# Kernel tuning notes

Measured on AMD Instinct MI355X. Metric: run time of the kernel, lower is better.

Reference implementation:

```python
import jax, jax.numpy as jnp
import numpy as np

B, N, DIM = 2, 512, 512
HEADS, DIM_HEAD, MAX_LEN = 8, 64, 1024


def _skew(QEr):
    # pad last dim on the left by 1, reshape (n, n+1) -> (n+1, n), drop first row
    padded = jnp.pad(QEr, ((0, 0), (0, 0), (0, 0), (1, 0)))
    b, h, r, c = padded.shape
    return padded.reshape(b, h, c, r)[:, :, 1:, :]


def _fft_multiply_parallel(A, x):
    # A: [b,h,n,n] decay matrix; x: [b,h,n,d]
    b, h, n, d = x.shape
    # y = [last column of A, first row of A] -> [b,h,2n]
    y = jnp.concatenate([A[:, :, :, -1], A[:, :, 0, :]], axis=-1)
    v = jnp.concatenate([x, jnp.zeros_like(x)], axis=-2)  # zero-pad rows n -> 2n
    # Faithful to the original torch code: fftn over ALL axes (incl. batch/head),
    # then ifft over the LAST axis only, then slice back to n rows.
    H = jnp.fft.fftn(y)[:, :, :, None] * jnp.fft.fftn(v)
    return jnp.fft.ifft(H)[:, :, :n, :]


def _forward(x, Wq, Wk, Wv, Er):
    b, n, _ = x.shape

    def split_heads(t):
        return t.reshape(b, n, HEADS, DIM_HEAD).transpose(0, 2, 1, 3)  # [b,h,n,d]

    q = split_heads(x @ Wq)
    k = split_heads(x @ Wk)
    v = split_heads(x @ Wv)
    # global (Frobenius) norm over the full tensor, as torch.norm(t)
    q = q / jnp.linalg.norm(q)
    k = k / jnp.linalg.norm(k)
    q_ = jax.nn.elu(q)
    k_ = jax.nn.elu(k)

    Er_t = Er[MAX_LEN - n:, :].T        # [d, n]
    QEr = q @ Er_t                       # [b,h,n,n]
    c = jnp.exp(_skew(QEr))              # relative-position decay, [b,h,n,n]

    a_1 = jnp.einsum('bhnx,bhny->bhnxy', k_, v).reshape(b, HEADS, n, DIM_HEAD * DIM_HEAD)
    d_2 = _fft_multiply_parallel(c, k_)                                   # [b,h,n,d] complex
    d_1 = _fft_multiply_parallel(c, a_1).reshape(b, HEADS, n, DIM_HEAD, DIM_HEAD)

    top = jnp.einsum('bhnx,bhnyz->bhnz', q_, d_1)    # complex [b,h,n,d]
    bottom = jnp.einsum('bhnx,bhny->bhny', q_, d_2)  # complex [b,h,n,d]
    return top / bottom


def setup_inputs() -> dict:
    key = jax.random.key(0)
    k1, k2, k3, k4, k5 = jax.random.split(key, 5)
    s = jnp.float32(1.0 / np.sqrt(DIM))
    return {
        'x': jax.random.normal(k1, (B, N, DIM), dtype=jnp.float32),
        'Wq': jax.random.normal(k2, (DIM, HEADS * DIM_HEAD), dtype=jnp.float32) * s,
        'Wk': jax.random.normal(k3, (DIM, HEADS * DIM_HEAD), dtype=jnp.float32) * s,
        'Wv': jax.random.normal(k4, (DIM, HEADS * DIM_HEAD), dtype=jnp.float32) * s,
        'Er': jax.random.normal(k5, (MAX_LEN, DIM_HEAD), dtype=jnp.float32),
    }


def reference(x, Wq, Wk, Wv, Er):
    return _forward(x, Wq, Wk, Wv, Er)
```

## Files before the change

### kernel.cpp

```cpp
#include <hip/hip_runtime.h>
#include <math.h>


#define DIMX 512
#define NPOS 512
#define PADIDX(m) ((m) + ((m) >> 4))

typedef unsigned short ushort_t;
typedef unsigned int uint_t;
typedef __bf16 bf16x8 __attribute__((ext_vector_type(8)));
typedef float floatx4 __attribute__((ext_vector_type(4)));

static __device__ inline ushort_t f2bf(float f) {
    uint_t u = __float_as_uint(f);
    u = u + 0x7FFFu + ((u >> 16) & 1u);
    return (ushort_t)(u >> 16);
}
static __device__ inline float bf2f(ushort_t h) {
    return __uint_as_float(((uint_t)h) << 16);
}

#define BFLY(lo, hi, tw) do {                                   \
    const float sr_ = (lo).x - (hi).x, si_ = (lo).y - (hi).y;   \
    (lo).x += (hi).x; (lo).y += (hi).y;                         \
    (hi).x = sr_ * (tw).x - si_ * (tw).y;                       \
    (hi).y = sr_ * (tw).y + si_ * (tw).x;                       \
} while (0)

__global__ __launch_bounds__(256)
void conv_kernel(const float* __restrict__ x,
                 const float* __restrict__ Wk, const float* __restrict__ Wv,
                 ushort_t* __restrict__ xh, ushort_t* __restrict__ xl,
                 ushort_t* __restrict__ wth, ushort_t* __restrict__ wtl,
                 float2* __restrict__ twd)
{
    const int blk = blockIdx.x;
    const int t = threadIdx.x;
    if (blk < 512) {
        const int idx4 = blk * 256 + t;
        const float4 v = ((const float4*)x)[idx4];
        const float vf[4] = {v.x, v.y, v.z, v.w};
        ushort_t h[4], l[4];
        #pragma unroll
        for (int e = 0; e < 4; ++e) {
            h[e] = f2bf(vf[e]);
            l[e] = f2bf(vf[e] - bf2f(h[e]));
        }
        ushort_t* ph = xh + (size_t)idx4 * 4;
        ushort_t* pl = xl + (size_t)idx4 * 4;
        #pragma unroll
        for (int e = 0; e < 4; ++e) { ph[e] = h[e]; pl[e] = l[e]; }
    } else if (blk < 1024) {
        __shared__ float tile[32][33];
        const int b2 = blk - 512;
        const int s  = b2 >> 8;
        const int kt = (b2 >> 4) & 15;
        const int nt = b2 & 15;
        const int c  = t & 31, r4 = t >> 5;
        const float* __restrict__ W = s ? Wv : Wk;
        #pragma unroll
        for (int i = 0; i < 4; ++i) {
            const int row = r4 + i * 8;
            tile[row][c] = W[(size_t)(kt * 32 + row) * 512 + nt * 32 + c];
        }
        __syncthreads();
        #pragma unroll
        for (int i = 0; i < 4; ++i) {
            const int nl = r4 + i * 8;
            const float v = tile[c][nl];
            const ushort_t h = f2bf(v);
            const ushort_t l = f2bf(v - bf2f(h));
            const size_t o = (size_t)(s * 512 + nt * 32 + nl) * 512 + kt * 32 + c;
            wth[o] = h;
            wtl[o] = l;
        }
    } else {
        const int jj = (blk - 1024) * 256 + t;
        double s, cc;
        sincos(-6.2831853071795864769 * (double)jj / 1024.0, &s, &cc);
        twd[jj] = make_float2((float)cc, (float)s);
    }
}

__global__ __launch_bounds__(256)
void gemm_mfma_kernel(const ushort_t* __restrict__ xh, const ushort_t* __restrict__ xl,
                      const ushort_t* __restrict__ wth, const ushort_t* __restrict__ wtl,
                      float* __restrict__ K, float* __restrict__ V,
                      float* __restrict__ partials)
{
    const int blk = blockIdx.x;
    const int ct = blk >> 5;
    const int rt = blk & 31;
    const int t = threadIdx.x;
    const int w = t >> 6, lane = t & 63;
    const int qd = lane >> 4, lm = lane & 15;
    const int mrow  = rt * 32 + (w >> 1) * 16 + lm;
    const int ncol0 = ct * 64 + (w & 1) * 32;
    const size_t aoff  = (size_t)mrow * 512 + qd * 8;
    const size_t boff0 = (size_t)(ncol0 + lm) * 512 + qd * 8;
    const size_t boff1 = (size_t)(ncol0 + 16 + lm) * 512 + qd * 8;

    floatx4 acc0 = {0.f, 0.f, 0.f, 0.f};
    floatx4 acc1 = {0.f, 0.f, 0.f, 0.f};

    #pragma unroll
    for (int ks = 0; ks < 16; ++ks) {
        const int k0 = ks * 32;
        const bf16x8 Ah  = *(const bf16x8*)&xh [aoff  + k0];
        const bf16x8 Al  = *(const bf16x8*)&xl [aoff  + k0];
        const bf16x8 B0h = *(const bf16x8*)&wth[boff0 + k0];
        const bf16x8 B0l = *(const bf16x8*)&wtl[boff0 + k0];
        const bf16x8 B1h = *(const bf16x8*)&wth[boff1 + k0];
        const bf16x8 B1l = *(const bf16x8*)&wtl[boff1 + k0];
        acc0 = __builtin_amdgcn_mfma_f32_16x16x32_bf16(Ah, B0h, acc0, 0, 0, 0);
        acc0 = __builtin_amdgcn_mfma_f32_16x16x32_bf16(Ah, B0l, acc0, 0, 0, 0);
        acc0 = __builtin_amdgcn_mfma_f32_16x16x32_bf16(Al, B0h, acc0, 0, 0, 0);
        acc1 = __builtin_amdgcn_mfma_f32_16x16x32_bf16(Ah, B1h, acc1, 0, 0, 0);
        acc1 = __builtin_amdgcn_mfma_f32_16x16x32_bf16(Ah, B1l, acc1, 0, 0, 0);
        acc1 = __builtin_amdgcn_mfma_f32_16x16x32_bf16(Al, B1h, acc1, 0, 0, 0);
    }

    __shared__ float red[4];
    float ss = 0.f;
    const int orow0 = rt * 32 + (w >> 1) * 16 + qd * 4;
    float* __restrict__ O = (ct < 8) ? K : V;
    const int cb = (ct < 8) ? 0 : 512;
    const int c0 = ncol0 + lm - cb;
    #pragma unroll
    for (int r = 0; r < 4; ++r) {
        const size_t row = orow0 + r;
        const float v0 = acc0[r], v1 = acc1[r];
        O[row * 512 + c0]      = v0;
        O[row * 512 + c0 + 16] = v1;
        if (ct < 8) ss += v0 * v0 + v1 * v1;
    }
    #pragma unroll
    for (int off = 32; off > 0; off >>= 1)
        ss += __shfl_down(ss, off, 64);
    if (lane == 0) red[w] = ss;
    __syncthreads();
    if (t == 0) partials[blk] = red[0] + red[1] + red[2] + red[3];
}

__device__ __constant__ float C8[8] = {
    1.f, 0.70710678118654752440f, 0.f, -0.70710678118654752440f,
   -1.f, -0.70710678118654752440f, 0.f, 0.70710678118654752440f };
__device__ __constant__ float S8[8] = {
    0.f, -0.70710678118654752440f, -1.f, -0.70710678118654752440f,
    0.f,  0.70710678118654752440f,  1.f,  0.70710678118654752440f };

__global__ __launch_bounds__(256)
void stage1_kernel(const float* __restrict__ K,
                   const float* __restrict__ V,
                   const float* __restrict__ partials,
                   float2* __restrict__ Gk,
                   float2* __restrict__ Gp)
{
    const int m = blockIdx.x;
    const int t = threadIdx.x;
    __shared__ float kk[2][8][64];
    __shared__ float pp[2][8][64];
    __shared__ float skp[16][4];
    __shared__ float sk[2][8];
    __shared__ float sred[4];

    float p = partials[t] + partials[t + 256];
    #pragma unroll
    for (int off = 32; off > 0; off >>= 1)
        p += __shfl_down(p, off, 64);
    if ((t & 63) == 0) sred[t >> 6] = p;
    __syncthreads();
    const float scale = (float)(1.0 / sqrt((double)sred[0] + (double)sred[1] +
                                           (double)sred[2] + (double)sred[3]));

    {
        const int e0 = t * 4;
        const int b = e0 >> 9, rem = e0 & 511, h = rem >> 6, z = rem & 63;
        const size_t src = (size_t)(b * 512 + m) * DIMX + h * 64 + z;
        const float4 kv4 = *(const float4*)&K[src];
        const float4 vv4 = *(const float4*)&V[src];
        const float kf[4] = {kv4.x, kv4.y, kv4.z, kv4.w};
        const float vf[4] = {vv4.x, vv4.y, vv4.z, vv4.w};
        #pragma unroll
        for (int e = 0; e < 4; ++e) {
            const float kv = kf[e] * scale;
            kk[b][h][z + e] = kv > 0.f ? kv : expm1f(kv);
            pp[b][h][z + e] = vf[e];
        }
    }
    __syncthreads();
    if (t < 64) {
        const int bh = t >> 2, q = t & 3;
        float s = 0.f;
        #pragma unroll
        for (int zz = 0; zz < 16; ++zz) s += kk[bh >> 3][bh & 7][q * 16 + zz];
        skp[bh][q] = s;
    }
    __syncthreads();
    if (t < 16) sk[t >> 3][t & 7] = skp[t][0] + skp[t][1] + skp[t][2] + skp[t][3];
    __syncthreads();
    for (int e = t; e < 1024; e += 256) {
        const int b = e >> 9, rem = e & 511, h = rem >> 6, z = rem & 63;
        pp[b][h][z] *= sk[b][h];
    }
    __syncthreads();

    for (int e2 = t; e2 < 512; e2 += 256) {
        const int be = e2 >> 5;
        const int zp = e2 & 31;
        const int beta = be >> 3, eta = be & 7;
        float4 rk, rp;
        #pragma unroll
        for (int zz = 0; zz < 2; ++zz) {
            const int z = zp * 2 + zz;
            float gkr = 0.f, gki = 0.f, gpr = 0.f, gpi = 0.f;
            #pragma unroll
            for (int b = 0; b < 2; ++b) {
                const float sgn = (beta & b) ? -1.f : 1.f;
                #pragma unroll
                for (int h = 0; h < 8; ++h) {
                    const int ph = (eta * h) & 7;
                    const float cr = C8[ph], ci = S8[ph];
                    const float a = kk[b][h][z] * sgn;
                    gkr = fmaf(a, cr, gkr); gki = fmaf(a, ci, gki);
                    const float p2 = pp[b][h][z] * sgn;
                    gpr = fmaf(p2, cr, gpr); gpi = fmaf(p2, ci, gpi);
                }
            }
            if (zz == 0) { rk.x = gkr; rk.y = gki; rp.x = gpr; rp.y = gpi; }
            else         { rk.z = gkr; rk.w = gki; rp.z = gpr; rp.w = gpi; }
        }
        const size_t o = ((size_t)be * NPOS + m) * 64 + zp * 2;
        *(float4*)&Gk[o] = rk;
        *(float4*)&Gp[o] = rp;
    }
}

__global__ __launch_bounds__(256)
void fft_div_kernel(const float2* __restrict__ Gk,
                    const float2* __restrict__ Gp,
                    const float2* __restrict__ twd,
                    float* __restrict__ out, int out_cplx)
{
    const int blk = blockIdx.x;
    const int j  = blk & 7;
    const int l  = (blk >> 3) & 3;
    const int be = blk >> 5;
    const int zg = j * 4 + l;
    const int t  = threadIdx.x;

    __shared__ float2 g[4][1088];
    __shared__ float2 w[544];

    for (int jj = t; jj < 512; jj += 256)
        w[PADIDX(jj)] = twd[jj];
    __syncthreads();

    for (int e = t; e < 1024; e += 256) {
        const int a = e >> 9;
        const int m = e & 511;
        const float4 v4 = *(const float4*)&(a ? Gp : Gk)[((size_t)be * NPOS + m) * 64 + zg * 2];
        const float2 v0 = make_float2(v4.x, v4.y);
        const float2 v1 = make_float2(v4.z, v4.w);
        const float2 tw = w[PADIDX(m)];
        g[a * 2 + 0][PADIDX(m)] = v0;
        g[a * 2 + 1][PADIDX(m)] = v1;
        g[a * 2 + 0][PADIDX(m + 512)] = make_float2(v0.x * tw.x - v0.y * tw.y,
                                                    v0.x * tw.y + v0.y * tw.x);
        g[a * 2 + 1][PADIDX(m + 512)] = make_float2(v1.x * tw.x - v1.y * tw.y,
                                                    v1.x * tw.y + v1.y * tw.x);
    }
    __syncthreads();

    const int wv   = t >> 6;
    const int lane = t & 63;

    #pragma unroll
    for (int q = 0; q < 2; ++q) {
        const int arr = wv;
        const int h   = q;
        const int jo  = lane;
        float2 f[8];
        #pragma unroll
        for (int k = 0; k < 8; ++k)
            f[k] = g[arr][PADIDX(h * 512 + jo + k * 64)];
        #pragma unroll
        for (int k = 0; k < 4; ++k) {
            const float2 tw = w[PADIDX(2 * jo + 128 * k)];
            BFLY(f[k], f[k + 4], tw);
        }
        {
            const float2 tw0 = w[PADIDX(4 * jo)];
            const float2 tw1 = w[PADIDX(4 * jo + 256)];
            BFLY(f[0], f[2], tw0); BFLY(f[1], f[3], tw1);
            BFLY(f[4], f[6], tw0); BFLY(f[5], f[7], tw1);
        }
        {
            const float2 tw = w[PADIDX(8 * jo)];
            BFLY(f[0], f[1], tw); BFLY(f[2], f[3], tw);
            BFLY(f[4], f[5], tw); BFLY(f[6], f[7], tw);
        }
        #pragma unroll
        for (int k = 0; k < 8; ++k)
            g[arr][PADIDX(h * 512 + jo + k * 64)] = f[k];
    }
    __syncthreads();

    #pragma unroll
    for (int q = 0; q < 2; ++q) {
        const int arr = wv;
        const int b64 = q * 8 + (lane >> 3);
        const int jo  = lane & 7;
        const int e0  = b64 * 64 + jo;
        float2 f[8];
        #pragma unroll
        for (int k = 0; k < 8; ++k)
            f[k] = g[arr][PADIDX(e0 + 8 * k)];
        #pragma unroll
        for (int k = 0; k < 4; ++k) {
            const float2 tw = w[PADIDX(16 * jo + 128 * k)];
            BFLY(f[k], f[k + 4], tw);
        }
        {
            const float2 tw0 = w[PADIDX(32 * jo)];
            const float2 tw1 = w[PADIDX(32 * jo + 256)];
            BFLY(f[0], f[2], tw0); BFLY(f[1], f[3], tw1);
            BFLY(f[4], f[6], tw0); BFLY(f[5], f[7], tw1);
        }
        {
            const float2 tw = w[PADIDX(64 * jo)];
            BFLY(f[0], f[1], tw); BFLY(f[2], f[3], tw);
            BFLY(f[4], f[5], tw); BFLY(f[6], f[7], tw);
        }
        #pragma unroll
        for (int k = 0; k < 8; ++k)
            g[arr][PADIDX(e0 + 8 * k)] = f[k];
    }
    __syncthreads();

    #pragma unroll
    for (int q = 0; q < 2; ++q) {
        const int arr = wv;
        const int b8  = q * 64 + lane;
        const int e0  = b8 * 8;
        float2 f[8];
        #pragma unroll
        for (int k = 0; k < 8; ++k)
            f[k] = g[arr][PADIDX(e0 + k)];
        BFLY(f[0], f[4], w[PADIDX(0)]);
        BFLY(f[1], f[5], w[PADIDX(128)]);
        BFLY(f[2], f[6], w[PADIDX(256)]);
        BFLY(f[3], f[7], w[PADIDX(384)]);
        {
            const float2 tw0 = w[PADIDX(0)];
            const float2 tw1 = w[PADIDX(256)];
            BFLY(f[0], f[2], tw0); BFLY(f[1], f[3], tw1);
            BFLY(f[4], f[6], tw0); BFLY(f[5], f[7], tw1);
        }
        f[0].x += f[1].x; f[0].y += f[1].y;
        f[2].x += f[3].x; f[2].y += f[3].y;
        f[4].x += f[5].x; f[4].y += f[5].y;
        f[6].x += f[7].x; f[6].y += f[7].y;
        g[arr][PADIDX(e0 + 0)] = f[0];
        g[arr][PADIDX(e0 + 2)] = f[2];
        g[arr][PADIDX(e0 + 4)] = f[4];
        g[arr][PADIDX(e0 + 6)] = f[6];
    }
    __syncthreads();

    for (int e2 = t; e2 < 512; e2 += 256) {
        const int i  = e2;
        const int pi = PADIDX(2 * i);
        const int mu = (int)(__brev((unsigned)i) >> 23);
        float4 res;
        #pragma unroll
        for (int zi = 0; zi < 2; ++zi) {
            const float2 D  = g[zi][pi];
            const float2 Nm = g[2 + zi][pi];
            const float inv = 1.f / (D.x * D.x + D.y * D.y);
            const float rr = (Nm.x * D.x + Nm.y * D.y) * inv;
            const float ri = (Nm.y * D.x - Nm.x * D.y) * inv;
            if (zi == 0) { res.x = rr; res.y = ri; }
            else         { res.z = rr; res.w = ri; }
        }
        const size_t o = ((size_t)be * NPOS + mu) * 64 + zg * 2;
        if (out_cplx) {
            *(float4*)&((float2*)out)[o] = res;
        } else {
            out[o]     = res.x;
            out[o + 1] = res.z;
        }
    }
}

__global__ __launch_bounds__(256)
void gemm_kv_kernel(const float* __restrict__ x,
                    const float* __restrict__ Wk,
                    const float* __restrict__ Wv,
                    float* __restrict__ K,
                    float* __restrict__ V,
                    float* __restrict__ partials)
{
    const int blk  = blockIdx.x;
    const int sel  = (blk >> 2) & 1;
    const int cg2  = blk & 3;
    const int rt   = blk >> 3;
    const int row0 = rt * 16;
    const int col0 = cg2 * 128;
    const int t    = threadIdx.x;
    const int tc   = t & 31;
    const int tr   = t >> 5;
    const float* __restrict__ W   = sel ? Wv : Wk;
    float* __restrict__       Out = sel ? V  : K;

    __shared__ float xs[16][DIMX];
    __shared__ float red[4];

    #pragma unroll
    for (int j = 0; j < 8; ++j) {
        const int f = t + j * 256;
        const int row = f >> 7, c4 = f & 127;
        *(float4*)&xs[row][c4 * 4] = *(const float4*)&x[(size_t)(row0 + row) * DIMX + c4 * 4];
    }
    __syncthreads();

    const float* Wb = W + col0 + tc * 4;
    float4 wA[8], wB[8];
    #pragma unroll
    for (int j = 0; j < 8; ++j) wA[j] = *(const float4*)&Wb[(size_t)(j) * DIMX];
    #pragma unroll
    for (int j = 0; j < 8; ++j) wB[j] = *(const float4*)&Wb[(size_t)(8 + j) * DIMX];

    float acc[2][4] = {{0,0,0,0},{0,0,0,0}};
    const int r0 = tr * 2;

    #define COMPUTE_CHUNK(WREG, CH)                                            \
        {   float4 xv0a = *(const float4*)&xs[r0][(CH) * 8];                   \
            float4 xv0b = *(const float4*)&xs[r0][(CH) * 8 + 4];               \
            float4 xv1a = *(const float4*)&xs[r0 + 1][(CH) * 8];               \
            float4 xv1b = *(const float4*)&xs[r0 + 1][(CH) * 8 + 4];           \
            _Pragma("unroll")                                                  \
            for (int kk = 0; kk < 4; ++kk) {                                   \
                const float x0 = (&xv0a.x)[kk], x1 = (&xv1a.x)[kk];            \
                _Pragma("unroll")                                              \
                for (int cc = 0; cc < 4; ++cc) {                               \
                    acc[0][cc] = fmaf(x0, (&WREG[kk].x)[cc], acc[0][cc]);      \
                    acc[1][cc] = fmaf(x1, (&WREG[kk].x)[cc], acc[1][cc]);      \
                } }                                                            \
            _Pragma("unroll")                                                  \
            for (int kk = 0; kk < 4; ++kk) {                                   \
                const float x0 = (&xv0b.x)[kk], x1 = (&xv1b.x)[kk];            \
                _Pragma("unroll")                                              \
                for (int cc = 0; cc < 4; ++cc) {                               \
                    acc[0][cc] = fmaf(x0, (&WREG[kk + 4].x)[cc], acc[0][cc]);  \
                    acc[1][cc] = fmaf(x1, (&WREG[kk + 4].x)[cc], acc[1][cc]);  \
                } } }

    for (int ch = 0; ch < 64; ch += 2) {
        COMPUTE_CHUNK(wA, ch)
        if (ch < 62) {
            #pragma unroll
            for (int j = 0; j < 8; ++j)
                wA[j] = *(const float4*)&Wb[(size_t)((ch + 2) * 8 + j) * DIMX];
        }
        COMPUTE_CHUNK(wB, ch + 1)
        if (ch < 62) {
            #pragma unroll
            for (int j = 0; j < 8; ++j)
                wB[j] = *(const float4*)&Wb[(size_t)((ch + 3) * 8 + j) * DIMX];
        }
    }
    #undef COMPUTE_CHUNK

    float ss = 0.f;
    #pragma unroll
    for (int i = 0; i < 2; ++i) {
        const int row = row0 + r0 + i;
        const float4 o = make_float4(acc[i][0], acc[i][1], acc[i][2], acc[i][3]);
        *(float4*)&Out[(size_t)row * DIMX + col0 + tc * 4] = o;
        ss += o.x * o.x + o.y * o.y + o.z * o.z + o.w * o.w;
    }
    if (sel == 0) {
        #pragma unroll
        for (int off = 32; off > 0; off >>= 1)
            ss += __shfl_down(ss, off, 64);
        if ((t & 63) == 0) red[t >> 6] = ss;
        __syncthreads();
        if (t == 0) partials[blk] = red[0] + red[1] + red[2] + red[3];
    } else {
        if (t == 0) partials[blk] = 0.f;
    }
}

__global__ __launch_bounds__(256)
void mdft_fallback_kernel(const float2* __restrict__ Gk,
                          const float2* __restrict__ Gp,
                          float* __restrict__ out,
                          int out_cplx)
{
    const int blk = blockIdx.x;
    const int be = blk >> 6, z = blk & 63;
    const int t = threadIdx.x;
    __shared__ float2 gk[512];
    __shared__ float2 gp[512];
    __shared__ float2 w[1024];

    for (int m = t; m < 512; m += 256) {
        const size_t idx = ((size_t)be * NPOS + m) * 64 + z;
        gk[m] = Gk[idx];
        gp[m] = Gp[idx];
    }
    for (int jj = t; jj < 1024; jj += 256) {
        double s, c;
        sincos(-6.2831853071795864769 * (double)jj / 1024.0, &s, &c);
        w[jj] = make_float2((float)c, (float)s);
    }
    __syncthreads();

    #pragma unroll
    for (int half = 0; half < 2; ++half) {
        const int mu = t + half * 256;
        double dr = 0.0, di = 0.0, nr = 0.0, ni = 0.0;
        int idx = 0;
        for (int m = 0; m < 512; ++m) {
            const float2 tw = w[idx];
            idx = (idx + mu) & 1023;
            const float2 a = gk[m];
            dr += (double)(a.x * tw.x - a.y * tw.y);
            di += (double)(a.x * tw.y + a.y * tw.x);
            const float2 p = gp[m];
            nr += (double)(p.x * tw.x - p.y * tw.y);
            ni += (double)(p.x * tw.y + p.y * tw.x);
        }
        const double dmag = dr * dr + di * di;
        const double orr = (nr * dr + ni * di) / dmag;
        const double oii = (ni * dr - nr * di) / dmag;
        const size_t o = ((size_t)be * NPOS + mu) * 64 + z;
        if (out_cplx) {
            out[2 * o]     = (float)orr;
            out[2 * o + 1] = (float)oii;
        } else {
            out[o] = (float)orr;
        }
    }
}

extern "C" void kernel_launch(void* const* d_in, const int* in_sizes, int n_in,
                              void* d_out, int out_size, void* d_ws, size_t ws_size,
                              hipStream_t stream)
{
    const float* x  = (const float*)d_in[0];
    const float* Wk = (const float*)d_in[2];
    const float* Wv = (const float*)d_in[3];
    float* out = (float*)d_out;

    char* ws = (char*)d_ws;
    float*  K    = (float*)(ws);
    float*  V    = (float*)(ws + (size_t)2097152);
    float2* Gk   = (float2*)(ws + (size_t)4194304);
    float*  part = (float*)(ws + (size_t)8388608);
    const int out_cplx = (out_size >= 2 * 2 * 8 * 512 * 64) ? 1 : 0;

    const bool ws_big = (ws_size >= (size_t)20971520);
    float2* Gp = ws_big ? (float2*)(ws + (size_t)8390656)
                        : (float2*)d_out;

    if (ws_big) {
        ushort_t* xh  = (ushort_t*)(ws + (size_t)16777216);
        ushort_t* xl  = (ushort_t*)(ws + (size_t)17825792);
        ushort_t* wth = (ushort_t*)(ws + (size_t)18874368);
        ushort_t* wtl = (ushort_t*)(ws + (size_t)19922944);
        float2*   twd = (float2*)(ws + (size_t)12584960);
        hipLaunchKernelGGL(conv_kernel, dim3(1026), dim3(256), 0, stream,
                           x, Wk, Wv, xh, xl, wth, wtl, twd);
        hipLaunchKernelGGL(gemm_mfma_kernel, dim3(512), dim3(256), 0, stream,
                           xh, xl, wth, wtl, K, V, part);
        hipLaunchKernelGGL(stage1_kernel, dim3(512), dim3(256), 0, stream,
                           K, V, part, Gk, Gp);
        hipLaunchKernelGGL(fft_div_kernel, dim3(512), dim3(256), 0, stream,
                           Gk, Gp, twd, out, out_cplx);
    } else {
        hipLaunchKernelGGL(gemm_kv_kernel, dim3(512), dim3(256), 0, stream,
                           x, Wk, Wv, K, V, part);
        hipLaunchKernelGGL(stage1_kernel, dim3(512), dim3(256), 0, stream,
                           K, V, part, Gk, Gp);
        hipLaunchKernelGGL(mdft_fallback_kernel, dim3(1024), dim3(256), 0, stream,
                           Gk, Gp, out, out_cplx);
    }
}
```

Measured before the change: 105.8 us.

## Transpose GEMM output, split ELU/scale prep, fuse head-DFT into FFT kernel

The GEMM now writes K and V transposed (feature-major, position-contiguous) with vectorized stores. A small prep kernel applies the norm scale, ELU and the per-head k-sum, and multiplies V by that sum. The 8x2 head/batch DFT that stage1 used to compute and write as Gk/Gp is now done directly inside the FFT kernel from the transposed buffers. This drops the large complex intermediate round-trip through global memory. Two __syncthreads in the FFT stages are removed, which is only safe if each thread reads only values it wrote itself.

```diff
diff --git a/kernel.cpp b/kernel.cpp
--- a/kernel.cpp
+++ b/kernel.cpp
@@ -85,7 +85,7 @@
 __global__ __launch_bounds__(256)
 void gemm_mfma_kernel(const ushort_t* __restrict__ xh, const ushort_t* __restrict__ xl,
                       const ushort_t* __restrict__ wth, const ushort_t* __restrict__ wtl,
-                      float* __restrict__ K, float* __restrict__ V,
+                      float* __restrict__ KT, float* __restrict__ VT,
                       float* __restrict__ partials)
 {
     const int blk = blockIdx.x;
@@ -121,18 +121,17 @@
     }
 
     __shared__ float red[4];
-    float ss = 0.f;
     const int orow0 = rt * 32 + (w >> 1) * 16 + qd * 4;
-    float* __restrict__ O = (ct < 8) ? K : V;
+    float* __restrict__ O = (ct < 8) ? KT : VT;
     const int cb = (ct < 8) ? 0 : 512;
     const int c0 = ncol0 + lm - cb;
-    #pragma unroll
-    for (int r = 0; r < 4; ++r) {
-        const size_t row = orow0 + r;
-        const float v0 = acc0[r], v1 = acc1[r];
-        O[row * 512 + c0]      = v0;
-        O[row * 512 + c0 + 16] = v1;
-        if (ct < 8) ss += v0 * v0 + v1 * v1;
+    *(floatx4*)&O[(size_t)c0 * 1024 + orow0]        = acc0;
+    *(floatx4*)&O[(size_t)(c0 + 16) * 1024 + orow0] = acc1;
+
+    float ss = 0.f;
+    if (ct < 8) {
+        #pragma unroll
+        for (int r = 0; r < 4; ++r) ss += acc0[r] * acc0[r] + acc1[r] * acc1[r];
     }
     #pragma unroll
     for (int off = 32; off > 0; off >>= 1)
@@ -140,6 +139,49 @@
     if (lane == 0) red[w] = ss;
     __syncthreads();
     if (t == 0) partials[blk] = red[0] + red[1] + red[2] + red[3];
+}
+
+__global__ __launch_bounds__(256)
+void skprep_kernel(const float* __restrict__ KT, const float* __restrict__ VT,
+                   const float* __restrict__ partials,
+                   float* __restrict__ KE, float* __restrict__ PT)
+{
+    const int blk = blockIdx.x;
+    const int h = blk >> 4;
+    const int col = (blk & 15) * 64 + (threadIdx.x & 63);
+    const int zq = threadIdx.x >> 6;
+    const int t = threadIdx.x;
+    __shared__ float sred[4];
+    __shared__ float skl[4][64];
+
+    float p = partials[t] + partials[t + 256];
+    #pragma unroll
+    for (int off = 32; off > 0; off >>= 1)
+        p += __shfl_down(p, off, 64);
+    if ((t & 63) == 0) sred[t >> 6] = p;
+    __syncthreads();
+    const float scale = (float)(1.0 / sqrt((double)sred[0] + (double)sred[1] +
+                                           (double)sred[2] + (double)sred[3]));
+
+    const int cbase = h * 64 + zq * 16;
+    float acc = 0.f;
+    #pragma unroll
+    for (int zz = 0; zz < 16; ++zz) {
+        const size_t o = (size_t)(cbase + zz) * 1024 + col;
+        const float kv = KT[o] * scale;
+        const float ke = kv > 0.f ? kv : expm1f(kv);
+        KE[o] = ke;
+        acc += ke;
+    }
+    skl[zq][t & 63] = acc;
+    __syncthreads();
+    const float sk = skl[0][t & 63] + skl[1][t & 63] +
+                     skl[2][t & 63] + skl[3][t & 63];
+    #pragma unroll
+    for (int zz = 0; zz < 16; ++zz) {
+        const size_t o = (size_t)(cbase + zz) * 1024 + col;
+        PT[o] = VT[o] * sk;
+    }
 }
 
 __device__ __constant__ float C8[8] = {
@@ -150,97 +192,10 @@
     0.f,  0.70710678118654752440f,  1.f,  0.70710678118654752440f };
 
 __global__ __launch_bounds__(256)
-void stage1_kernel(const float* __restrict__ K,
-                   const float* __restrict__ V,
-                   const float* __restrict__ partials,
-                   float2* __restrict__ Gk,
-                   float2* __restrict__ Gp)
-{
-    const int m = blockIdx.x;
-    const int t = threadIdx.x;
-    __shared__ float kk[2][8][64];
-    __shared__ float pp[2][8][64];
-    __shared__ float skp[16][4];
-    __shared__ float sk[2][8];
-    __shared__ float sred[4];
-
-    float p = partials[t] + partials[t + 256];
-    #pragma unroll
-    for (int off = 32; off > 0; off >>= 1)
-        p += __shfl_down(p, off, 64);
-    if ((t & 63) == 0) sred[t >> 6] = p;
-    __syncthreads();
-    const float scale = (float)(1.0 / sqrt((double)sred[0] + (double)sred[1] +
-                                           (double)sred[2] + (double)sred[3]));
-
-    {
-        const int e0 = t * 4;
-        const int b = e0 >> 9, rem = e0 & 511, h = rem >> 6, z = rem & 63;
-        const size_t src = (size_t)(b * 512 + m) * DIMX + h * 64 + z;
-        const float4 kv4 = *(const float4*)&K[src];
-        const float4 vv4 = *(const float4*)&V[src];
-        const float kf[4] = {kv4.x, kv4.y, kv4.z, kv4.w};
-        const float vf[4] = {vv4.x, vv4.y, vv4.z, vv4.w};
-        #pragma unroll
-        for (int e = 0; e < 4; ++e) {
-            const float kv = kf[e] * scale;
-            kk[b][h][z + e] = kv > 0.f ? kv : expm1f(kv);
-            pp[b][h][z + e] = vf[e];
-        }
-    }
-    __syncthreads();
-    if (t < 64) {
-        const int bh = t >> 2, q = t & 3;
-        float s = 0.f;
-        #pragma unroll
-        for (int zz = 0; zz < 16; ++zz) s += kk[bh >> 3][bh & 7][q * 16 + zz];
-        skp[bh][q] = s;
-    }
-    __syncthreads();
-    if (t < 16) sk[t >> 3][t & 7] = skp[t][0] + skp[t][1] + skp[t][2] + skp[t][3];
-    __syncthreads();
-    for (int e = t; e < 1024; e += 256) {
-        const int b = e >> 9, rem = e & 511, h = rem >> 6, z = rem & 63;
-        pp[b][h][z] *= sk[b][h];
-    }
-    __syncthreads();
-
-    for (int e2 = t; e2 < 512; e2 += 256) {
-        const int be = e2 >> 5;
-        const int zp = e2 & 31;
-        const int beta = be >> 3, eta = be & 7;
-        float4 rk, rp;
-        #pragma unroll
-        for (int zz = 0; zz < 2; ++zz) {
-            const int z = zp * 2 + zz;
-            float gkr = 0.f, gki = 0.f, gpr = 0.f, gpi = 0.f;
-            #pragma unroll
-            for (int b = 0; b < 2; ++b) {
-                const float sgn = (beta & b) ? -1.f : 1.f;
-                #pragma unroll
-                for (int h = 0; h < 8; ++h) {
-                    const int ph = (eta * h) & 7;
-                    const float cr = C8[ph], ci = S8[ph];
-                    const float a = kk[b][h][z] * sgn;
-                    gkr = fmaf(a, cr, gkr); gki = fmaf(a, ci, gki);
-                    const float p2 = pp[b][h][z] * sgn;
-                    gpr = fmaf(p2, cr, gpr); gpi = fmaf(p2, ci, gpi);
-                }
-            }
-            if (zz == 0) { rk.x = gkr; rk.y = gki; rp.x = gpr; rp.y = gpi; }
-            else         { rk.z = gkr; rk.w = gki; rp.z = gpr; rp.w = gpi; }
-        }
-        const size_t o = ((size_t)be * NPOS + m) * 64 + zp * 2;
-        *(float4*)&Gk[o] = rk;
-        *(float4*)&Gp[o] = rp;
-    }
-}
-
-__global__ __launch_bounds__(256)
-void fft_div_kernel(const float2* __restrict__ Gk,
-                    const float2* __restrict__ Gp,
-                    const float2* __restrict__ twd,
-                    float* __restrict__ out, int out_cplx)
+void fft_fused_kernel(const float* __restrict__ KE,
+                      const float* __restrict__ PT,
+                      const float2* __restrict__ twd,
+                      float* __restrict__ out, int out_cplx)
 {
     const int blk = blockIdx.x;
     const int j  = blk & 7;
@@ -256,24 +211,60 @@
         w[PADIDX(jj)] = twd[jj];
     __syncthreads();
 
-    for (int e = t; e < 1024; e += 256) {
-        const int a = e >> 9;
-        const int m = e & 511;
-        const float4 v4 = *(const float4*)&(a ? Gp : Gk)[((size_t)be * NPOS + m) * 64 + zg * 2];
-        const float2 v0 = make_float2(v4.x, v4.y);
-        const float2 v1 = make_float2(v4.z, v4.w);
-        const float2 tw = w[PADIDX(m)];
-        g[a * 2 + 0][PADIDX(m)] = v0;
-        g[a * 2 + 1][PADIDX(m)] = v1;
-        g[a * 2 + 0][PADIDX(m + 512)] = make_float2(v0.x * tw.x - v0.y * tw.y,
-                                                    v0.x * tw.y + v0.y * tw.x);
-        g[a * 2 + 1][PADIDX(m + 512)] = make_float2(v1.x * tw.x - v1.y * tw.y,
-                                                    v1.x * tw.y + v1.y * tw.x);
-    }
-    __syncthreads();
-
     const int wv   = t >> 6;
     const int lane = t & 63;
+    const int beta = be >> 3, eta = be & 7;
+    const int m0 = wv * 128 + lane * 2;
+
+    float gkr[2][2] = {{0.f,0.f},{0.f,0.f}};
+    float gki[2][2] = {{0.f,0.f},{0.f,0.f}};
+    float gpr[2][2] = {{0.f,0.f},{0.f,0.f}};
+    float gpi[2][2] = {{0.f,0.f},{0.f,0.f}};
+
+    #pragma unroll
+    for (int b = 0; b < 2; ++b) {
+        const float sgn = (beta & b) ? -1.f : 1.f;
+        #pragma unroll
+        for (int h = 0; h < 8; ++h) {
+            const int ph = (eta * h) & 7;
+            const float cr = C8[ph], ci = S8[ph];
+            const size_t base = (size_t)(h * 64 + zg * 2) * 1024 + b * 512 + m0;
+            const float2 ke0 = *(const float2*)&KE[base];
+            const float2 ke1 = *(const float2*)&KE[base + 1024];
+            const float2 pt0 = *(const float2*)&PT[base];
+            const float2 pt1 = *(const float2*)&PT[base + 1024];
+            #define ACC_TAP(zi, mi, kv, pv)                              \
+            {   const float a_ = (kv) * sgn;                             \
+                gkr[zi][mi] = fmaf(a_, cr, gkr[zi][mi]);                 \
+                gki[zi][mi] = fmaf(a_, ci, gki[zi][mi]);                 \
+                const float p_ = (pv) * sgn;                             \
+                gpr[zi][mi] = fmaf(p_, cr, gpr[zi][mi]);                 \
+                gpi[zi][mi] = fmaf(p_, ci, gpi[zi][mi]); }
+            ACC_TAP(0, 0, ke0.x, pt0.x)
+            ACC_TAP(0, 1, ke0.y, pt0.y)
+            ACC_TAP(1, 0, ke1.x, pt1.x)
+            ACC_TAP(1, 1, ke1.y, pt1.y)
+            #undef ACC_TAP
+        }
+    }
+
+    #pragma unroll
+    for (int mi = 0; mi < 2; ++mi) {
+        const int m = m0 + mi;
+        const float2 tw = w[PADIDX(m)];
+        #pragma unroll
+        for (int zi = 0; zi < 2; ++zi) {
+            const float2 vk = make_float2(gkr[zi][mi], gki[zi][mi]);
+            const float2 vp = make_float2(gpr[zi][mi], gpi[zi][mi]);
+            g[zi][PADIDX(m)]     = vk;
+            g[2 + zi][PADIDX(m)] = vp;
+            g[zi][PADIDX(m + 512)] = make_float2(vk.x * tw.x - vk.y * tw.y,
+                                                 vk.x * tw.y + vk.y * tw.x);
+            g[2 + zi][PADIDX(m + 512)] = make_float2(vp.x * tw.x - vp.y * tw.y,
+                                                     vp.x * tw.y + vp.y * tw.x);
+        }
+    }
+    __syncthreads();
 
     #pragma unroll
     for (int q = 0; q < 2; ++q) {
@@ -304,7 +295,6 @@
         for (int k = 0; k < 8; ++k)
             g[arr][PADIDX(h * 512 + jo + k * 64)] = f[k];
     }
-    __syncthreads();
 
     #pragma unroll
     for (int q = 0; q < 2; ++q) {
@@ -336,7 +326,6 @@
         for (int k = 0; k < 8; ++k)
             g[arr][PADIDX(e0 + 8 * k)] = f[k];
     }
-    __syncthreads();
 
     #pragma unroll
     for (int q = 0; q < 2; ++q) {
@@ -417,8 +406,8 @@
     __shared__ float red[4];
 
     #pragma unroll
-    for (int j = 0; j < 8; ++j) {
-        const int f = t + j * 256;
+    for (int jj = 0; jj < 8; ++jj) {
+        const int f = t + jj * 256;
         const int row = f >> 7, c4 = f & 127;
         *(float4*)&xs[row][c4 * 4] = *(const float4*)&x[(size_t)(row0 + row) * DIMX + c4 * 4];
     }
@@ -427,9 +416,9 @@
     const float* Wb = W + col0 + tc * 4;
     float4 wA[8], wB[8];
     #pragma unroll
-    for (int j = 0; j < 8; ++j) wA[j] = *(const float4*)&Wb[(size_t)(j) * DIMX];
-    #pragma unroll
-    for (int j = 0; j < 8; ++j) wB[j] = *(const float4*)&Wb[(size_t)(8 + j) * DIMX];
+    for (int jj = 0; jj < 8; ++jj) wA[jj] = *(const float4*)&Wb[(size_t)(jj) * DIMX];
+    #pragma unroll
+    for (int jj = 0; jj < 8; ++jj) wB[jj] = *(const float4*)&Wb[(size_t)(8 + jj) * DIMX];
 
     float acc[2][4] = {{0,0,0,0},{0,0,0,0}};
     const int r0 = tr * 2;
@@ -460,14 +449,14 @@
         COMPUTE_CHUNK(wA, ch)
         if (ch < 62) {
             #pragma unroll
-            for (int j = 0; j < 8; ++j)
-                wA[j] = *(const float4*)&Wb[(size_t)((ch + 2) * 8 + j) * DIMX];
+            for (int jj = 0; jj < 8; ++jj)
+                wA[jj] = *(const float4*)&Wb[(size_t)((ch + 2) * 8 + jj) * DIMX];
         }
         COMPUTE_CHUNK(wB, ch + 1)
         if (ch < 62) {
             #pragma unroll
-            for (int j = 0; j < 8; ++j)
-                wB[j] = *(const float4*)&Wb[(size_t)((ch + 3) * 8 + j) * DIMX];
+            for (int jj = 0; jj < 8; ++jj)
+                wB[jj] = *(const float4*)&Wb[(size_t)((ch + 3) * 8 + jj) * DIMX];
         }
     }
     #undef COMPUTE_CHUNK
@@ -489,6 +478,93 @@
         if (t == 0) partials[blk] = red[0] + red[1] + red[2] + red[3];
     } else {
         if (t == 0) partials[blk] = 0.f;
+    }
+}
+
+__global__ __launch_bounds__(256)
+void stage1_kernel(const float* __restrict__ K,
+                   const float* __restrict__ V,
+                   const float* __restrict__ partials,
+                   float2* __restrict__ Gk,
+                   float2* __restrict__ Gp)
+{
+    const int m = blockIdx.x;
+    const int t = threadIdx.x;
+    __shared__ float kk[2][8][64];
+    __shared__ float pp[2][8][64];
+    __shared__ float skp[16][4];
+    __shared__ float sk[2][8];
+    __shared__ float sred[4];
+
+    float p = partials[t] + partials[t + 256];
+    #pragma unroll
+    for (int off = 32; off > 0; off >>= 1)
+        p += __shfl_down(p, off, 64);
+    if ((t & 63) == 0) sred[t >> 6] = p;
+    __syncthreads();
+    const float scale = (float)(1.0 / sqrt((double)sred[0] + (double)sred[1] +
+                                           (double)sred[2] + (double)sred[3]));
+
+    {
+        const int e0 = t * 4;
+        const int b = e0 >> 9, rem = e0 & 511, h = rem >> 6, z = rem & 63;
+        const size_t src = (size_t)(b * 512 + m) * DIMX + h * 64 + z;
+        const float4 kv4 = *(const float4*)&K[src];
+        const float4 vv4 = *(const float4*)&V[src];
+        const float kf[4] = {kv4.x, kv4.y, kv4.z, kv4.w};
+        const float vf[4] = {vv4.x, vv4.y, vv4.z, vv4.w};
+        #pragma unroll
+        for (int e = 0; e < 4; ++e) {
+            const float kv = kf[e] * scale;
+            kk[b][h][z + e] = kv > 0.f ? kv : expm1f(kv);
+            pp[b][h][z + e] = vf[e];
+        }
+    }
+    __syncthreads();
+    if (t < 64) {
+        const int bh = t >> 2, q = t & 3;
+        float s = 0.f;
+        #pragma unroll
+        for (int zz = 0; zz < 16; ++zz) s += kk[bh >> 3][bh & 7][q * 16 + zz];
+        skp[bh][q] = s;
+    }
+    __syncthreads();
+    if (t < 16) sk[t >> 3][t & 7] = skp[t][0] + skp[t][1] + skp[t][2] + skp[t][3];
+    __syncthreads();
+    for (int e = t; e < 1024; e += 256) {
+        const int b = e >> 9, rem = e & 511, h = rem >> 6, z = rem & 63;
+        pp[b][h][z] *= sk[b][h];
+    }
+    __syncthreads();
+
+    for (int e2 = t; e2 < 512; e2 += 256) {
+        const int be = e2 >> 5;
+        const int zp = e2 & 31;
+        const int beta = be >> 3, eta = be & 7;
+        float4 rk, rp;
+        #pragma unroll
+        for (int zz = 0; zz < 2; ++zz) {
+            const int z = zp * 2 + zz;
+            float gkr = 0.f, gki = 0.f, gpr = 0.f, gpi = 0.f;
+            #pragma unroll
+            for (int b = 0; b < 2; ++b) {
+                const float sgn = (beta & b) ? -1.f : 1.f;
+                #pragma unroll
+                for (int h = 0; h < 8; ++h) {
+                    const int ph = (eta * h) & 7;
+                    const float cr = C8[ph], ci = S8[ph];
+                    const float a = kk[b][h][z] * sgn;
+                    gkr = fmaf(a, cr, gkr); gki = fmaf(a, ci, gki);
+                    const float p2 = pp[b][h][z] * sgn;
+                    gpr = fmaf(p2, cr, gpr); gpi = fmaf(p2, ci, gpi);
+                }
+            }
+            if (zz == 0) { rk.x = gkr; rk.y = gki; rp.x = gpr; rp.y = gpi; }
+            else         { rk.z = gkr; rk.w = gki; rp.z = gpr; rp.w = gpi; }
+        }
+        const size_t o = ((size_t)be * NPOS + m) * 64 + zp * 2;
+        *(float4*)&Gk[o] = rk;
+        *(float4*)&Gp[o] = rp;
     }
 }
 
@@ -528,9 +604,9 @@
             const float2 a = gk[m];
             dr += (double)(a.x * tw.x - a.y * tw.y);
             di += (double)(a.x * tw.y + a.y * tw.x);
-            const float2 p = gp[m];
-            nr += (double)(p.x * tw.x - p.y * tw.y);
-            ni += (double)(p.x * tw.y + p.y * tw.x);
+            const float2 p2 = gp[m];
+            nr += (double)(p2.x * tw.x - p2.y * tw.y);
+            ni += (double)(p2.x * tw.y + p2.y * tw.x);
         }
         const double dmag = dr * dr + di * di;
         const double orr = (nr * dr + ni * di) / dmag;
@@ -555,17 +631,16 @@
     float* out = (float*)d_out;
 
     char* ws = (char*)d_ws;
-    float*  K    = (float*)(ws);
-    float*  V    = (float*)(ws + (size_t)2097152);
-    float2* Gk   = (float2*)(ws + (size_t)4194304);
     float*  part = (float*)(ws + (size_t)8388608);
     const int out_cplx = (out_size >= 2 * 2 * 8 * 512 * 64) ? 1 : 0;
 
     const bool ws_big = (ws_size >= (size_t)20971520);
-    float2* Gp = ws_big ? (float2*)(ws + (size_t)8390656)
-                        : (float2*)d_out;
 
     if (ws_big) {
+        float*    KT  = (float*)(ws);
+        float*    VT  = (float*)(ws + (size_t)2097152);
+        float*    KE  = (float*)(ws + (size_t)4194304);
+        float*    PT  = (float*)(ws + (size_t)6291456);
         ushort_t* xh  = (ushort_t*)(ws + (size_t)16777216);
         ushort_t* xl  = (ushort_t*)(ws + (size_t)17825792);
         ushort_t* wth = (ushort_t*)(ws + (size_t)18874368);
@@ -574,12 +649,16 @@
         hipLaunchKernelGGL(conv_kernel, dim3(1026), dim3(256), 0, stream,
                            x, Wk, Wv, xh, xl, wth, wtl, twd);
         hipLaunchKernelGGL(gemm_mfma_kernel, dim3(512), dim3(256), 0, stream,
-                           xh, xl, wth, wtl, K, V, part);
-        hipLaunchKernelGGL(stage1_kernel, dim3(512), dim3(256), 0, stream,
-                           K, V, part, Gk, Gp);
-        hipLaunchKernelGGL(fft_div_kernel, dim3(512), dim3(256), 0, stream,
-                           Gk, Gp, twd, out, out_cplx);
+                           xh, xl, wth, wtl, KT, VT, part);
+        hipLaunchKernelGGL(skprep_kernel, dim3(128), dim3(256), 0, stream,
+                           KT, VT, part, KE, PT);
+        hipLaunchKernelGGL(fft_fused_kernel, dim3(512), dim3(256), 0, stream,
+                           KE, PT, twd, out, out_cplx);
     } else {
+        float*  K  = (float*)(ws);
+        float*  V  = (float*)(ws + (size_t)2097152);
+        float2* Gk = (float2*)(ws + (size_t)4194304);
+        float2* Gp = (float2*)d_out;
         hipLaunchKernelGGL(gemm_kv_kernel, dim3(512), dim3(256), 0, stream,
                            x, Wk, Wv, K, V, part);
         hipLaunchKernelGGL(stage1_kernel, dim3(512), dim3(256), 0, stream,
```

Result: slower. 108.8 us (+2.8%).
